# Performance work log

Measured on AMD Instinct MI355X. Metric: run time of the kernel, lower is better.

## Reference

```python
import jax, jax.numpy as jnp
import numpy as np

N_NODES = 50000
N_EDGES = 800000
IN_DIM = 128
OUT_DIM = 128
NEG_SLOPE = 0.01  # F.leaky_relu default


def setup_inputs() -> dict:
    key = jax.random.key(0)
    k_h, k_src, k_dst, k_w, k_as, k_ad = jax.random.split(key, 6)
    h = jax.random.normal(k_h, (N_NODES, IN_DIM), dtype=jnp.float32)
    src = jax.random.randint(k_src, (N_EDGES,), 0, N_NODES, dtype=jnp.int32)
    dst = jax.random.randint(k_dst, (N_EDGES,), 0, N_NODES, dtype=jnp.int32)
    # fc weight: xavier_normal with relu gain; stored as [in, out] for h @ W
    gain = float(np.sqrt(2.0))
    std_w = gain * np.sqrt(2.0 / (IN_DIM + OUT_DIM))
    W = jax.random.normal(k_w, (IN_DIM, OUT_DIM), dtype=jnp.float32) * std_w
    # attn weight [1, 2*out] split into src/dst halves (concat@a == z_s@a_s + z_d@a_d)
    std_a = gain * np.sqrt(2.0 / (2 * OUT_DIM + 1))
    a_src = jax.random.normal(k_as, (OUT_DIM,), dtype=jnp.float32) * std_a
    a_dst = jax.random.normal(k_ad, (OUT_DIM,), dtype=jnp.float32) * std_a
    return {"h": h, "src": src, "dst": dst, "W": W, "a_src": a_src, "a_dst": a_dst}


def reference(h, src, dst, W, a_src, a_dst):
    n = h.shape[0]
    z = h @ W                                   # [N, D]
    # edge attention: leaky_relu(attn(concat[z_src, z_dst]))
    e = z[src] @ a_src + z[dst] @ a_dst         # [E]
    e = jnp.where(e >= 0, e, NEG_SLOPE * e)
    # segment softmax over incoming edges of each dst node
    m = jax.ops.segment_max(e, dst, num_segments=n)    # [N]
    m = jnp.where(jnp.isfinite(m), m, 0.0)             # guard zero-in-degree nodes
    ex = jnp.exp(e - m[dst])                            # [E]
    denom = jax.ops.segment_sum(ex, dst, num_segments=n)
    denom = jnp.where(denom > 0, denom, 1.0)
    alpha = ex / denom[dst]                             # [E]
    # weighted scatter-sum of source features
    out = jax.ops.segment_sum(alpha[:, None] * z[src], dst, num_segments=n)  # [N, D]
    return out
```

## Files before the change

### kernel.cpp

```cpp
#include <hip/hip_runtime.h>
#include <math.h>

#define DIM 128
#define NEG_SLOPE 0.01f
#define CAP 64

typedef __attribute__((ext_vector_type(8))) short bf16x8;
typedef __attribute__((ext_vector_type(4))) float f32x4;
typedef unsigned int uint;
typedef unsigned short ushort;

static __device__ __forceinline__ uint f2bf(float x) {
  uint u = __float_as_uint(x);
  return (u + 0x7fffu + ((u >> 16) & 1u)) >> 16;
}

__global__ __launch_bounds__(256) void init_k(
    const float* __restrict__ W, ushort* __restrict__ Wt16,
    int* __restrict__ cur, int n)
{
  const int t = threadIdx.x, b = blockIdx.x;
  if (b == 0) {
    const float4* W4 = (const float4*)W;
    #pragma unroll
    for (int it = 0; it < 16; ++it) {
      int i = t + it * 256;
      int k = i >> 5, n4 = (i & 31) * 4;
      float4 v = W4[i];
      Wt16[(n4 + 0) * 128 + k] = (ushort)f2bf(v.x);
      Wt16[(n4 + 1) * 128 + k] = (ushort)f2bf(v.y);
      Wt16[(n4 + 2) * 128 + k] = (ushort)f2bf(v.z);
      Wt16[(n4 + 3) * 128 + k] = (ushort)f2bf(v.w);
    }
  } else {
    int i = (b - 1) * 256 + t;
    if (i < n) cur[i] = 0;
  }
}

__global__ __launch_bounds__(256, 4) void mega(
    const float* __restrict__ W,
    const float* __restrict__ a_src, const float* __restrict__ a_dst,
    const float* __restrict__ h,
    const int* __restrict__ src, const int* __restrict__ dst,
    const ushort* __restrict__ Wt16,
    float* __restrict__ s, float* __restrict__ d,
    int* __restrict__ cur, ushort* __restrict__ bucket,
    uint* __restrict__ zb,
    int n, int E, int nfill, int nsd)
{
  __shared__ __align__(16) ushort smem[64 * 136];
  const int t = threadIdx.x;
  const int b = blockIdx.x;

  if (b < nfill) {
    int base = b * 1024 + t;
    int sj[4], dj[4], c[4];
    #pragma unroll
    for (int u = 0; u < 4; ++u) {
      int i = base + u * 256;
      dj[u] = -1;
      if (i < E) { sj[u] = src[i]; dj[u] = dst[i]; }
    }
    #pragma unroll
    for (int u = 0; u < 4; ++u)
      if (dj[u] >= 0) c[u] = atomicAdd(&cur[dj[u]], 1);
    #pragma unroll
    for (int u = 0; u < 4; ++u)
      if (dj[u] >= 0 && c[u] < CAP)
        bucket[dj[u] * CAP + c[u]] = (ushort)sj[u];
    return;
  }

  if (b < nfill + nsd) {
    float* vec = (float*)smem;
    {
      const float* row = W + (size_t)(t & 127) * DIM;
      const float* a = (t < 128) ? a_src : a_dst;
      float acc = 0.f;
      #pragma unroll 16
      for (int j = 0; j < DIM; ++j) acc = fmaf(row[j], a[j], acc);
      vec[(t >> 7) * DIM + (t & 127)] = acc;
    }
    __syncthreads();
    int i = (b - nfill) * 256 + t;
    if (i < n) {
      const float4* h4 = (const float4*)(h + (size_t)i * DIM);
      float sp = 0.f, dp = 0.f;
      #pragma unroll 8
      for (int c2 = 0; c2 < 32; ++c2) {
        float4 v = h4[c2];
        sp = fmaf(v.x, vec[c2*4+0], fmaf(v.y, vec[c2*4+1],
             fmaf(v.z, vec[c2*4+2], fmaf(v.w, vec[c2*4+3], sp))));
        dp = fmaf(v.x, vec[DIM+c2*4+0], fmaf(v.y, vec[DIM+c2*4+1],
             fmaf(v.z, vec[DIM+c2*4+2], fmaf(v.w, vec[DIM+c2*4+3], dp))));
      }
      s[i] = sp; d[i] = dp;
    }
    return;
  }

  const int g = b - nfill - nsd;
  const int lane = t & 63, wv = t >> 6;
  const int row0 = g * 64;
  ushort* hb = smem;

  {
    const float4* h4 = (const float4*)h;
    #pragma unroll
    for (int it = 0; it < 8; ++it) {
      int i = t + it * 256;
      int r = i >> 5, c4 = i & 31;
      float4 v = make_float4(0.f, 0.f, 0.f, 0.f);
      if (row0 + r < n) v = h4[(size_t)(row0 + r) * 32 + c4];
      uint2 pk;
      pk.x = f2bf(v.x) | (f2bf(v.y) << 16);
      pk.y = f2bf(v.z) | (f2bf(v.w) << 16);
      *(uint2*)&hb[r * 136 + c4 * 4] = pk;
    }
  }
  __syncthreads();

  f32x4 acc[8];
  #pragma unroll
  for (int c2 = 0; c2 < 8; ++c2) acc[c2] = (f32x4){0.f, 0.f, 0.f, 0.f};

  const int m = lane & 15, quad = lane >> 4;
  const ushort* arow = &hb[(wv * 16 + m) * 136 + quad * 8];
  const ushort* bb = Wt16 + (size_t)m * 128 + quad * 8;

  #pragma unroll
  for (int ks = 0; ks < 4; ++ks) {
    bf16x8 af = *(const bf16x8*)(arow + ks * 32);
    #pragma unroll
    for (int c2 = 0; c2 < 8; ++c2) {
      bf16x8 bf = *(const bf16x8*)(bb + c2 * 2048 + ks * 32);
      acc[c2] = __builtin_amdgcn_mfma_f32_16x16x32_bf16(af, bf, acc[c2], 0, 0, 0);
    }
  }

  __syncthreads();
  #pragma unroll
  for (int c2 = 0; c2 < 8; ++c2) {
    int col = c2 * 16 + m;
    #pragma unroll
    for (int reg = 0; reg < 4; ++reg) {
      int r = wv * 16 + quad * 4 + reg;
      hb[r * 136 + col] = (ushort)f2bf(acc[c2][reg]);
    }
  }
  __syncthreads();
  #pragma unroll
  for (int it = 0; it < 4; ++it) {
    int i = t + it * 256;
    int r = i >> 4, c8 = i & 15;
    int rg = row0 + r;
    if (rg < n) {
      uint4 v = *(uint4*)&hb[r * 136 + c8 * 8];
      *(uint4*)&zb[(size_t)rg * 64 + c8 * 4] = v;
    }
  }
}

__global__ __launch_bounds__(256) void gat_node(
    const uint* __restrict__ zb, const float* __restrict__ s,
    const float* __restrict__ d, const int* __restrict__ cur,
    const ushort* __restrict__ bucket, float* __restrict__ out, int n)
{
  int wave = threadIdx.x >> 6;
  int lane = threadIdx.x & 63;
  int node = blockIdx.x * 4 + wave;
  if (node >= n) return;

  int cnt = min(cur[node], CAP);
  float2* out2 = (float2*)out;
  if (cnt <= 0) {
    out2[(size_t)node * 64 + lane] = make_float2(0.f, 0.f);
    return;
  }

  float dn = d[node];
  int sj = 0; float w = 0.f;
  if (lane < cnt) {
    sj = (int)bucket[node * CAP + lane];
    float e = s[sj] + dn;
    e = (e >= 0.f) ? e : NEG_SLOPE * e;
    w = __expf(e);
  }
  float denom = w;
  #pragma unroll
  for (int o = 32; o > 0; o >>= 1) denom += __shfl_xor(denom, o, 64);

  float2 acc = make_float2(0.f, 0.f);
  int tt = 0;
  for (; tt + 8 <= cnt; tt += 8) {
    uint zv[8]; float wt[8];
    #pragma unroll
    for (int u = 0; u < 8; ++u) {
      int st = __shfl(sj, tt + u, 64);
      zv[u] = zb[(size_t)st * 64 + lane];
      wt[u] = __shfl(w, tt + u, 64);
    }
    #pragma unroll
    for (int u = 0; u < 8; ++u) {
      acc.x = fmaf(wt[u], __uint_as_float(zv[u] << 16), acc.x);
      acc.y = fmaf(wt[u], __uint_as_float(zv[u] & 0xffff0000u), acc.y);
    }
  }
  for (; tt < cnt; ++tt) {
    int st = __shfl(sj, tt, 64);
    uint u = zb[(size_t)st * 64 + lane];
    float wt = __shfl(w, tt, 64);
    acc.x = fmaf(wt, __uint_as_float(u << 16), acc.x);
    acc.y = fmaf(wt, __uint_as_float(u & 0xffff0000u), acc.y);
  }
  float inv = 1.f / denom;
  out2[(size_t)node * 64 + lane] = make_float2(acc.x * inv, acc.y * inv);
}

extern "C" void kernel_launch(void* const* d_in, const int* in_sizes, int n_in,
                              void* d_out, int out_size, void* d_ws, size_t ws_size,
                              hipStream_t stream)
{
  const float* h     = (const float*)d_in[0];
  const int*   src   = (const int*)d_in[1];
  const int*   dst   = (const int*)d_in[2];
  const float* W     = (const float*)d_in[3];
  const float* a_src = (const float*)d_in[4];
  const float* a_dst = (const float*)d_in[5];
  float* out = (float*)d_out;

  const int n = in_sizes[0] / DIM;
  const int E = in_sizes[1];

  char* ws = (char*)d_ws;
  uint* zb       = (uint*)ws;   ws += (size_t)n * 64 * 4;
  float* s       = (float*)ws;  ws += (size_t)n * 4;
  float* d       = (float*)ws;  ws += (size_t)n * 4;
  int* cur       = (int*)ws;    ws += (size_t)n * 4;
  ushort* Wt16   = (ushort*)ws; ws += (size_t)DIM * DIM * 2;
  ushort* bucket = (ushort*)ws;

  const int nsd   = (n + 255) / 256;
  const int nfill = (E + 1023) / 1024;
  const int ngemm = (n + 63) / 64;
  const int nzero = (n + 255) / 256;

  init_k<<<1 + nzero, 256, 0, stream>>>(W, Wt16, cur, n);
  mega<<<nfill + nsd + ngemm, 256, 0, stream>>>(
      W, a_src, a_dst, h, src, dst, Wt16, s, d, cur, bucket, zb,
      n, E, nfill, nsd);
  gat_node<<<(n + 3) / 4, 256, 0, stream>>>(zb, s, d, cur, bucket, out, n);
}
```

Measured before the change: 186.6 us.

## Fuse edge fill, attention scores and GEMM into one block role

Each block of the combined kernel now does three jobs at once: it buckets 1024 edges, computes the per-node src/dst attention scores from the h tile it already loads for the GEMM, and runs the bf16 MFMA projection. The W·a vectors and the W transpose are precomputed in init_k, with the transpose spread over 16 blocks. This drops the second full read of h done by the separate score blocks and the heterogeneous block dispatch, and it overlaps the atomic latency with the h loads. In exchange each thread uses more registers and does wave shuffle reductions. The edge and GEMM roles also need extra bounds handling whenever the edge-block and row-block counts differ.

```diff
diff --git a/kernel.cpp b/kernel.cpp
--- a/kernel.cpp
+++ b/kernel.cpp
@@ -16,114 +16,98 @@
 }
 
 __global__ __launch_bounds__(256) void init_k(
-    const float* __restrict__ W, ushort* __restrict__ Wt16,
+    const float* __restrict__ W,
+    const float* __restrict__ a_src, const float* __restrict__ a_dst,
+    ushort* __restrict__ Wt16, float* __restrict__ g_vec,
     int* __restrict__ cur, int n)
 {
   const int t = threadIdx.x, b = blockIdx.x;
   if (b == 0) {
+    const float* row = W + (size_t)(t & 127) * DIM;
+    const float* a = (t < 128) ? a_src : a_dst;
+    float acc = 0.f;
+    #pragma unroll 16
+    for (int j = 0; j < DIM; ++j) acc = fmaf(row[j], a[j], acc);
+    g_vec[t] = acc;
+  } else if (b <= 16) {
     const float4* W4 = (const float4*)W;
-    #pragma unroll
-    for (int it = 0; it < 16; ++it) {
-      int i = t + it * 256;
-      int k = i >> 5, n4 = (i & 31) * 4;
-      float4 v = W4[i];
-      Wt16[(n4 + 0) * 128 + k] = (ushort)f2bf(v.x);
-      Wt16[(n4 + 1) * 128 + k] = (ushort)f2bf(v.y);
-      Wt16[(n4 + 2) * 128 + k] = (ushort)f2bf(v.z);
-      Wt16[(n4 + 3) * 128 + k] = (ushort)f2bf(v.w);
-    }
+    int i = (b - 1) * 256 + t;
+    int k = i >> 5, n4 = (i & 31) * 4;
+    float4 v = W4[i];
+    Wt16[(n4 + 0) * 128 + k] = (ushort)f2bf(v.x);
+    Wt16[(n4 + 1) * 128 + k] = (ushort)f2bf(v.y);
+    Wt16[(n4 + 2) * 128 + k] = (ushort)f2bf(v.z);
+    Wt16[(n4 + 3) * 128 + k] = (ushort)f2bf(v.w);
   } else {
-    int i = (b - 1) * 256 + t;
+    int i = (b - 17) * 256 + t;
     if (i < n) cur[i] = 0;
   }
 }
 
-__global__ __launch_bounds__(256, 4) void mega(
-    const float* __restrict__ W,
-    const float* __restrict__ a_src, const float* __restrict__ a_dst,
-    const float* __restrict__ h,
+__global__ __launch_bounds__(256) void gemm_fill(
+    const float* __restrict__ h, const ushort* __restrict__ Wt16,
+    const float* __restrict__ g_vec,
     const int* __restrict__ src, const int* __restrict__ dst,
-    const ushort* __restrict__ Wt16,
+    int* __restrict__ cur, ushort* __restrict__ bucket,
     float* __restrict__ s, float* __restrict__ d,
-    int* __restrict__ cur, ushort* __restrict__ bucket,
     uint* __restrict__ zb,
-    int n, int E, int nfill, int nsd)
-{
-  __shared__ __align__(16) ushort smem[64 * 136];
+    int n, int E)
+{
+  __shared__ __align__(16) ushort hb[64 * 136];
   const int t = threadIdx.x;
+  const int lane = t & 63, wv = t >> 6;
   const int b = blockIdx.x;
-
-  if (b < nfill) {
-    int base = b * 1024 + t;
-    int sj[4], dj[4], c[4];
+  const int row0 = b * 64;
+
+  int sj[4], dj[4], cc[4];
+  {
+    int ebase = b * 1024 + t;
     #pragma unroll
     for (int u = 0; u < 4; ++u) {
-      int i = base + u * 256;
+      int i = ebase + u * 256;
       dj[u] = -1;
       if (i < E) { sj[u] = src[i]; dj[u] = dst[i]; }
     }
     #pragma unroll
     for (int u = 0; u < 4; ++u)
-      if (dj[u] >= 0) c[u] = atomicAdd(&cur[dj[u]], 1);
-    #pragma unroll
-    for (int u = 0; u < 4; ++u)
-      if (dj[u] >= 0 && c[u] < CAP)
-        bucket[dj[u] * CAP + c[u]] = (ushort)sj[u];
-    return;
-  }
-
-  if (b < nfill + nsd) {
-    float* vec = (float*)smem;
-    {
-      const float* row = W + (size_t)(t & 127) * DIM;
-      const float* a = (t < 128) ? a_src : a_dst;
-      float acc = 0.f;
-      #pragma unroll 16
-      for (int j = 0; j < DIM; ++j) acc = fmaf(row[j], a[j], acc);
-      vec[(t >> 7) * DIM + (t & 127)] = acc;
-    }
-    __syncthreads();
-    int i = (b - nfill) * 256 + t;
-    if (i < n) {
-      const float4* h4 = (const float4*)(h + (size_t)i * DIM);
-      float sp = 0.f, dp = 0.f;
-      #pragma unroll 8
-      for (int c2 = 0; c2 < 32; ++c2) {
-        float4 v = h4[c2];
-        sp = fmaf(v.x, vec[c2*4+0], fmaf(v.y, vec[c2*4+1],
-             fmaf(v.z, vec[c2*4+2], fmaf(v.w, vec[c2*4+3], sp))));
-        dp = fmaf(v.x, vec[DIM+c2*4+0], fmaf(v.y, vec[DIM+c2*4+1],
-             fmaf(v.z, vec[DIM+c2*4+2], fmaf(v.w, vec[DIM+c2*4+3], dp))));
-      }
-      s[i] = sp; d[i] = dp;
-    }
-    return;
-  }
-
-  const int g = b - nfill - nsd;
-  const int lane = t & 63, wv = t >> 6;
-  const int row0 = g * 64;
-  ushort* hb = smem;
-
+      if (dj[u] >= 0) cc[u] = atomicAdd(&cur[dj[u]], 1);
+  }
+
+  const int c4 = t & 31;
+  const float4 v0 = ((const float4*)g_vec)[c4];
+  const float4 v1 = ((const float4*)g_vec)[32 + c4];
   {
     const float4* h4 = (const float4*)h;
     #pragma unroll
     for (int it = 0; it < 8; ++it) {
-      int i = t + it * 256;
-      int r = i >> 5, c4 = i & 31;
+      int r = (t >> 5) + it * 8;
       float4 v = make_float4(0.f, 0.f, 0.f, 0.f);
       if (row0 + r < n) v = h4[(size_t)(row0 + r) * 32 + c4];
       uint2 pk;
       pk.x = f2bf(v.x) | (f2bf(v.y) << 16);
       pk.y = f2bf(v.z) | (f2bf(v.w) << 16);
       *(uint2*)&hb[r * 136 + c4 * 4] = pk;
-    }
-  }
+      float spv = fmaf(v.x, v0.x, fmaf(v.y, v0.y, fmaf(v.z, v0.z, v.w * v0.w)));
+      float dpv = fmaf(v.x, v1.x, fmaf(v.y, v1.y, fmaf(v.z, v1.z, v.w * v1.w)));
+      #pragma unroll
+      for (int o = 16; o > 0; o >>= 1) {
+        spv += __shfl_xor(spv, o, 64);
+        dpv += __shfl_xor(dpv, o, 64);
+      }
+      if ((t & 31) == 0 && row0 + r < n) { s[row0 + r] = spv; d[row0 + r] = dpv; }
+    }
+  }
+
+  #pragma unroll
+  for (int u = 0; u < 4; ++u)
+    if (dj[u] >= 0 && cc[u] < CAP)
+      bucket[dj[u] * CAP + cc[u]] = (ushort)sj[u];
+
   __syncthreads();
 
   f32x4 acc[8];
   #pragma unroll
-  for (int c2 = 0; c2 < 8; ++c2) acc[c2] = (f32x4){0.f, 0.f, 0.f, 0.f};
+  for (int c = 0; c < 8; ++c) acc[c] = (f32x4){0.f, 0.f, 0.f, 0.f};
 
   const int m = lane & 15, quad = lane >> 4;
   const ushort* arow = &hb[(wv * 16 + m) * 136 + quad * 8];
@@ -133,20 +117,20 @@
   for (int ks = 0; ks < 4; ++ks) {
     bf16x8 af = *(const bf16x8*)(arow + ks * 32);
     #pragma unroll
-    for (int c2 = 0; c2 < 8; ++c2) {
-      bf16x8 bf = *(const bf16x8*)(bb + c2 * 2048 + ks * 32);
-      acc[c2] = __builtin_amdgcn_mfma_f32_16x16x32_bf16(af, bf, acc[c2], 0, 0, 0);
+    for (int c = 0; c < 8; ++c) {
+      bf16x8 bf = *(const bf16x8*)(bb + c * 2048 + ks * 32);
+      acc[c] = __builtin_amdgcn_mfma_f32_16x16x32_bf16(af, bf, acc[c], 0, 0, 0);
     }
   }
 
   __syncthreads();
   #pragma unroll
-  for (int c2 = 0; c2 < 8; ++c2) {
-    int col = c2 * 16 + m;
+  for (int c = 0; c < 8; ++c) {
+    int col = c * 16 + m;
     #pragma unroll
     for (int reg = 0; reg < 4; ++reg) {
       int r = wv * 16 + quad * 4 + reg;
-      hb[r * 136 + col] = (ushort)f2bf(acc[c2][reg]);
+      hb[r * 136 + col] = (ushort)f2bf(acc[c][reg]);
     }
   }
   __syncthreads();
@@ -239,16 +223,16 @@
   float* d       = (float*)ws;  ws += (size_t)n * 4;
   int* cur       = (int*)ws;    ws += (size_t)n * 4;
   ushort* Wt16   = (ushort*)ws; ws += (size_t)DIM * DIM * 2;
+  float* g_vec   = (float*)ws;  ws += 256 * 4;
   ushort* bucket = (ushort*)ws;
 
-  const int nsd   = (n + 255) / 256;
-  const int nfill = (E + 1023) / 1024;
+  const int nzero = (n + 255) / 256;
   const int ngemm = (n + 63) / 64;
-  const int nzero = (n + 255) / 256;
-
-  init_k<<<1 + nzero, 256, 0, stream>>>(W, Wt16, cur, n);
-  mega<<<nfill + nsd + ngemm, 256, 0, stream>>>(
-      W, a_src, a_dst, h, src, dst, Wt16, s, d, cur, bucket, zb,
-      n, E, nfill, nsd);
+  const int nedge = (E + 1023) / 1024;
+  const int nblk  = ngemm > nedge ? ngemm : nedge;
+
+  init_k<<<17 + nzero, 256, 0, stream>>>(W, a_src, a_dst, Wt16, g_vec, cur, n);
+  gemm_fill<<<nblk, 256, 0, stream>>>(
+      h, Wt16, g_vec, src, dst, cur, bucket, s, d, zb, n, E);
   gat_node<<<(n + 3) / 4, 256, 0, stream>>>(zb, s, d, cur, bucket, out, n);
 }
```

Measured after the change: 181.6 us. -2.7%, faster.
